# Performance work log

Hardware: AMD Instinct MI355X
Metric: run time of the kernel (lower is better)

Reference implementation:

```python
import jax, jax.numpy as jnp
import numpy as np

N = 8192      # source grid points
M = 8192      # output grid points
NB = 16       # n_basis
WIDTH = 32    # int(n_basis * enhancement)
EPS = 1e-4
LOG2 = 0.6931471805599453


def log_cosh(x):
    a = jnp.abs(x)
    return a + jnp.log1p(jnp.exp(-2.0 * a)) - LOG2


def setup_inputs() -> dict:
    key = jax.random.key(0)
    ks = jax.random.split(key, 9)
    rho = jax.random.uniform(ks[0], (N,), minval=0.05, maxval=2.0)
    gamma = jax.random.uniform(ks[1], (N,), minval=0.01, maxval=1.0)
    coords = jax.random.normal(ks[2], (N, 3)) * 5.0
    weights = jax.random.uniform(ks[3], (N,), minval=0.0, maxval=0.1)
    out_coords = jax.random.normal(ks[4], (M, 3)) * 5.0
    # field_embed params: Linear(1 -> WIDTH), Linear(WIDTH -> NB)
    w1 = jax.random.normal(ks[5], (1, WIDTH)) * 1.0
    b1 = jax.random.normal(ks[6], (WIDTH,)) * 0.1
    w2 = jax.random.normal(ks[7], (WIDTH, NB)) / np.sqrt(WIDTH)
    b2 = jax.random.normal(ks[8], (NB,)) * 0.1
    return {"rho": rho, "gamma": gamma, "coords": coords, "weights": weights,
            "out_coords": out_coords, "w1": w1, "b1": b1, "w2": w2, "b2": b2}


def _field_embed(x, w1, b1, w2, b2):
    # x: (..., 1) -> (..., NB)
    return jnp.tanh(x @ w1 + b1) @ w2 + b2


def reference(rho, gamma, coords, weights, out_coords, w1, b1, w2, b2):
    # rescaled (reduced) density gradient s^2 = gamma / (4 (3 pi^2)^{2/3} rho^{8/3})
    s2 = gamma / (4.0 * (3.0 * jnp.pi ** 2) ** (2.0 / 3.0) * rho ** (8.0 / 3.0))
    x = jnp.log(s2 + EPS)[:, None]                     # (N, 1)
    exponent = log_cosh(_field_embed(x, w1, b1, w2, b2))  # (N, NB)
    heg_scale = log_cosh(_field_embed(jnp.zeros((1, 1), rho.dtype), w1, b1, w2, b2)) ** 1.5  # (1, NB)
    beta = jnp.pi * (rho[:, None] / 2.0) ** (2.0 / 3.0) * exponent  # (N, NB)
    wrho = weights * rho                                # (N,)

    # all-pairs squared distances (M, N), computed once
    d2 = (jnp.sum(out_coords ** 2, axis=1)[:, None]
          + jnp.sum(coords ** 2, axis=1)[None, :]
          - 2.0 * out_coords @ coords.T)
    d2 = jnp.maximum(d2, 0.0)

    # KeOps Genred: y[i, b] = sum_j exp(-beta[j, b] * d2[i, j]) * wrho[j]
    # scan over the (small, fixed) basis axis so only one (M, N) kernel slice lives at a time
    def body(carry, beta_b):                            # beta_b: (N,)
        yb = jnp.exp(-d2 * beta_b[None, :]) @ wrho      # (M,)
        return carry, yb

    _, ys = jax.lax.scan(body, 0, beta.T)               # (NB, M)
    return ys.T * heg_scale                             # (M, NB)
```

## Files before the change

kernel.cpp:

```cpp
#include <hip/hip_runtime.h>
#include <hip/hip_bf16.h>


#define N_PTS 8192
#define M_PTS 8192
#define NBASIS 16
#define WIDTH 32

typedef float v2f __attribute__((ext_vector_type(2)));

__device__ __forceinline__ float exp2_hw(float x) { return __builtin_amdgcn_exp2f(x); }
__device__ __forceinline__ float log2_hw(float x) { return __builtin_amdgcn_logf(x); }

__device__ __forceinline__ float fast_tanh(float z) {
    float a = fabsf(z);
    float t = __expf(-2.0f * a);
    float r = (1.0f - t) / (1.0f + t);
    return copysignf(r, z);
}

__device__ __forceinline__ float log_cosh_f(float x) {
    float a = fabsf(x);
    return a + __logf(1.0f + __expf(-2.0f * a)) - 0.6931471805599453f;
}

__global__ __launch_bounds__(64)
void cg_prep(const float* __restrict__ rho,
             const float* __restrict__ gamma,
             const float* __restrict__ coords,
             const float* __restrict__ weights,
             const float* __restrict__ w1,
             const float* __restrict__ b1,
             const float* __restrict__ w2,
             const float* __restrict__ b2,
             float4* __restrict__ cw,
             float4* __restrict__ bnq,
             float* __restrict__ hegf)
{
    const float PI_F = 3.14159265358979323846f;
    const float LOG2E = 1.4426950408889634f;

    __shared__ float s_w1[WIDTH], s_b1[WIDTH], s_w2[WIDTH * NBASIS], s_b2[NBASIS];
    int t = threadIdx.x;
    if (t < WIDTH) { s_w1[t] = w1[t]; s_b1[t] = b1[t]; }
    if (t < NBASIS) s_b2[t] = b2[t];
    #pragma unroll
    for (int k = 0; k < 8; ++k) s_w2[t + 64 * k] = w2[t + 64 * k];
    __syncthreads();

    int j = blockIdx.x * 64 + t;
    {
        float r = rho[j];
        float g = gamma[j];
        const float c83 = 38.28312007948569f;
        float r83 = exp2_hw(2.6666666667f * log2_hw(r));
        float s2 = g / (c83 * r83);
        float x = __logf(s2 + 1e-4f);

        float emb[NBASIS];
        #pragma unroll
        for (int b = 0; b < NBASIS; ++b) emb[b] = s_b2[b];
        #pragma unroll 4
        for (int w = 0; w < WIDTH; ++w) {
            float h = fast_tanh(fmaf(x, s_w1[w], s_b1[w]));
            #pragma unroll
            for (int b = 0; b < NBASIS; ++b)
                emb[b] = fmaf(h, s_w2[w * NBASIS + b], emb[b]);
        }
        float pref = PI_F * exp2_hw(0.6666666667f * log2_hw(0.5f * r));
        float scale = -LOG2E * pref;
        #pragma unroll
        for (int q = 0; q < 4; ++q) {
            bnq[q * N_PTS + j] = make_float4(scale * log_cosh_f(emb[4 * q + 0]),
                                             scale * log_cosh_f(emb[4 * q + 1]),
                                             scale * log_cosh_f(emb[4 * q + 2]),
                                             scale * log_cosh_f(emb[4 * q + 3]));
        }

        cw[j] = make_float4(coords[j * 3 + 0],
                            coords[j * 3 + 1],
                            coords[j * 3 + 2],
                            weights[j] * r);
    }

    if (blockIdx.x == 0 && t == 0) {
        float emb0[NBASIS];
        #pragma unroll
        for (int b = 0; b < NBASIS; ++b) emb0[b] = s_b2[b];
        for (int w = 0; w < WIDTH; ++w) {
            float h = fast_tanh(s_b1[w]);
            #pragma unroll
            for (int b = 0; b < NBASIS; ++b)
                emb0[b] = fmaf(h, s_w2[w * NBASIS + b], emb0[b]);
        }
        #pragma unroll
        for (int b = 0; b < NBASIS; ++b) {
            float lc = fmaxf(log_cosh_f(emb0[b]), 0.0f);
            hegf[b] = lc * sqrtf(lc);
        }
    }
}

__global__ __launch_bounds__(256, 4)
void cg_pairs(const float* __restrict__ oc,
              const float4* __restrict__ cw,
              const float4* __restrict__ bnq,
              const float* __restrict__ hegf,
              float* __restrict__ out)
{
    int wave = (blockIdx.x << 2) | (threadIdx.x >> 6);
    int lane = threadIdx.x & 63;
    int i0 = wave << 1;
    int i1 = i0 | 1;

    v2f oxv = { oc[i0 * 3 + 0], oc[i1 * 3 + 0] };
    v2f oyv = { oc[i0 * 3 + 1], oc[i1 * 3 + 1] };
    v2f ozv = { oc[i0 * 3 + 2], oc[i1 * 3 + 2] };

    v2f acc[NBASIS];
    #pragma unroll
    for (int b = 0; b < NBASIS; ++b) acc[b] = (v2f)0.0f;

    #pragma unroll 2
    for (int k = 0; k < N_PTS / 64; ++k) {
        int j = (k << 6) | lane;
        float4 c = cw[j];
        v2f dx = oxv - c.x;
        v2f dy = oyv - c.y;
        v2f dz = ozv - c.z;
        v2f d2 = dx * dx + dy * dy + dz * dz;
        #pragma unroll
        for (int q = 0; q < 4; ++q) {
            float4 b4 = bnq[q * N_PTS + j];
            v2f p0 = b4.x * d2;
            v2f p1 = b4.y * d2;
            v2f p2 = b4.z * d2;
            v2f p3 = b4.w * d2;
            v2f e0 = { exp2_hw(p0.x), exp2_hw(p0.y) };
            v2f e1 = { exp2_hw(p1.x), exp2_hw(p1.y) };
            v2f e2 = { exp2_hw(p2.x), exp2_hw(p2.y) };
            v2f e3 = { exp2_hw(p3.x), exp2_hw(p3.y) };
            acc[q * 4 + 0] += e0 * c.w;
            acc[q * 4 + 1] += e1 * c.w;
            acc[q * 4 + 2] += e2 * c.w;
            acc[q * 4 + 3] += e3 * c.w;
        }
    }

    #pragma unroll
    for (int m = 1; m < 64; m <<= 1) {
        #pragma unroll
        for (int b = 0; b < NBASIS; ++b) {
            v2f other = { __shfl_xor(acc[b].x, m, 64),
                          __shfl_xor(acc[b].y, m, 64) };
            acc[b] += other;
        }
    }

    if (lane == 0) {
        #pragma unroll
        for (int b = 0; b < NBASIS; ++b) {
            float h = hegf[b];
            out[i0 * NBASIS + b] = acc[b].x * h;
            out[i1 * NBASIS + b] = acc[b].y * h;
        }
    }
}

extern "C" void kernel_launch(void* const* d_in, const int* in_sizes, int n_in,
                              void* d_out, int out_size, void* d_ws, size_t ws_size,
                              hipStream_t stream) {
    const float* rho        = (const float*)d_in[0];
    const float* gamma      = (const float*)d_in[1];
    const float* coords     = (const float*)d_in[2];
    const float* weights    = (const float*)d_in[3];
    const float* out_coords = (const float*)d_in[4];
    const float* w1         = (const float*)d_in[5];
    const float* b1         = (const float*)d_in[6];
    const float* w2         = (const float*)d_in[7];
    const float* b2         = (const float*)d_in[8];

    char* ws = (char*)d_ws;
    float4* cw   = (float4*)(ws);
    float4* bnq  = (float4*)(ws + (128 << 10));
    float*  hegf = (float*) (ws + (640 << 10));

    cg_prep<<<N_PTS / 64, 64, 0, stream>>>(rho, gamma, coords, weights,
                                           w1, b1, w2, b2,
                                           cw, bnq, hegf);

    cg_pairs<<<M_PTS / 8, 256, 0, stream>>>(out_coords, cw, bnq, hegf,
                                            (float*)d_out);
}
```

Baseline: 189.7 us.

## Offload a quarter of exp2 to FMA polynomial and software-prefetch pair loads

Splits the transcendental load in the pairwise kernel: 12 of 16 basis exponentials still use the hardware exp2 instruction, while the last 4 use a degree-6 polynomial with exponent bit construction on packed FMA units. This is meant to balance the transcendental pipe against the vector ALU. It also double-buffers the coordinate and basis loads one iteration ahead and vectorizes the final output stores. The polynomial adds many ALU instructions and some register pressure, and may lose slight accuracy for very negative arguments where it clamps to tiny values.

```diff
diff --git a/kernel.cpp b/kernel.cpp
--- a/kernel.cpp
+++ b/kernel.cpp
@@ -22,6 +22,24 @@
 __device__ __forceinline__ float log_cosh_f(float x) {
     float a = fabsf(x);
     return a + __logf(1.0f + __expf(-2.0f * a)) - 0.6931471805599453f;
+}
+
+__device__ __forceinline__ v2f exp2_pair_poly(v2f p) {
+    v2f n = { rintf(p.x), rintf(p.y) };
+    v2f r = p - n;
+    int nx = (int)n.x;
+    int ny = (int)n.y;
+    nx = nx < -127 ? -127 : nx;
+    ny = ny < -127 ? -127 : ny;
+    v2f s = { __builtin_bit_cast(float, (nx + 127) << 23),
+              __builtin_bit_cast(float, (ny + 127) << 23) };
+    v2f q = r * 1.535336188319500e-4f + 1.339887440266574e-3f;
+    q = q * r + 9.618437357674640e-3f;
+    q = q * r + 5.550332471162809e-2f;
+    q = q * r + 2.402264791363012e-1f;
+    q = q * r + 6.931472028550421e-1f;
+    q = q * r + 1.0f;
+    return q * s;
 }
 
 __global__ __launch_bounds__(64)
@@ -121,31 +139,62 @@
     #pragma unroll
     for (int b = 0; b < NBASIS; ++b) acc[b] = (v2f)0.0f;
 
-    #pragma unroll 2
-    for (int k = 0; k < N_PTS / 64; ++k) {
-        int j = (k << 6) | lane;
-        float4 c = cw[j];
+    auto hwq = [&](const float4& B, v2f d2, v2f w, int o) {
+        v2f p0 = B.x * d2;
+        v2f p1 = B.y * d2;
+        v2f p2 = B.z * d2;
+        v2f p3 = B.w * d2;
+        v2f e0 = { exp2_hw(p0.x), exp2_hw(p0.y) };
+        v2f e1 = { exp2_hw(p1.x), exp2_hw(p1.y) };
+        v2f e2 = { exp2_hw(p2.x), exp2_hw(p2.y) };
+        v2f e3 = { exp2_hw(p3.x), exp2_hw(p3.y) };
+        acc[o + 0] += e0 * w;
+        acc[o + 1] += e1 * w;
+        acc[o + 2] += e2 * w;
+        acc[o + 3] += e3 * w;
+    };
+    auto polyq = [&](const float4& B, v2f d2, v2f w, int o) {
+        v2f p0 = B.x * d2;
+        v2f p1 = B.y * d2;
+        v2f p2 = B.z * d2;
+        v2f p3 = B.w * d2;
+        acc[o + 0] += exp2_pair_poly(p0) * w;
+        acc[o + 1] += exp2_pair_poly(p1) * w;
+        acc[o + 2] += exp2_pair_poly(p2) * w;
+        acc[o + 3] += exp2_pair_poly(p3) * w;
+    };
+    auto body = [&](const float4& c, const float4& B0, const float4& B1,
+                    const float4& B2, const float4& B3) {
         v2f dx = oxv - c.x;
         v2f dy = oyv - c.y;
         v2f dz = ozv - c.z;
         v2f d2 = dx * dx + dy * dy + dz * dz;
-        #pragma unroll
-        for (int q = 0; q < 4; ++q) {
-            float4 b4 = bnq[q * N_PTS + j];
-            v2f p0 = b4.x * d2;
-            v2f p1 = b4.y * d2;
-            v2f p2 = b4.z * d2;
-            v2f p3 = b4.w * d2;
-            v2f e0 = { exp2_hw(p0.x), exp2_hw(p0.y) };
-            v2f e1 = { exp2_hw(p1.x), exp2_hw(p1.y) };
-            v2f e2 = { exp2_hw(p2.x), exp2_hw(p2.y) };
-            v2f e3 = { exp2_hw(p3.x), exp2_hw(p3.y) };
-            acc[q * 4 + 0] += e0 * c.w;
-            acc[q * 4 + 1] += e1 * c.w;
-            acc[q * 4 + 2] += e2 * c.w;
-            acc[q * 4 + 3] += e3 * c.w;
-        }
-    }
+        v2f w = (v2f)c.w;
+        hwq(B0, d2, w, 0);
+        hwq(B1, d2, w, 4);
+        hwq(B2, d2, w, 8);
+        polyq(B3, d2, w, 12);
+    };
+
+    float4 c_c  = cw[lane];
+    float4 b0_c = bnq[0 * N_PTS + lane];
+    float4 b1_c = bnq[1 * N_PTS + lane];
+    float4 b2_c = bnq[2 * N_PTS + lane];
+    float4 b3_c = bnq[3 * N_PTS + lane];
+
+    for (int k = 0; k < N_PTS / 64 - 1; ++k) {
+        int jn = ((k + 1) << 6) | lane;
+        float4 c_n  = cw[jn];
+        float4 b0_n = bnq[0 * N_PTS + jn];
+        float4 b1_n = bnq[1 * N_PTS + jn];
+        float4 b2_n = bnq[2 * N_PTS + jn];
+        float4 b3_n = bnq[3 * N_PTS + jn];
+
+        body(c_c, b0_c, b1_c, b2_c, b3_c);
+
+        c_c = c_n; b0_c = b0_n; b1_c = b1_n; b2_c = b2_n; b3_c = b3_n;
+    }
+    body(c_c, b0_c, b1_c, b2_c, b3_c);
 
     #pragma unroll
     for (int m = 1; m < 64; m <<= 1) {
@@ -158,11 +207,18 @@
     }
 
     if (lane == 0) {
-        #pragma unroll
-        for (int b = 0; b < NBASIS; ++b) {
-            float h = hegf[b];
-            out[i0 * NBASIS + b] = acc[b].x * h;
-            out[i1 * NBASIS + b] = acc[b].y * h;
+        float4* o0 = (float4*)(out + i0 * NBASIS);
+        float4* o1 = (float4*)(out + i1 * NBASIS);
+        #pragma unroll
+        for (int q = 0; q < 4; ++q) {
+            float h0 = hegf[4 * q + 0];
+            float h1 = hegf[4 * q + 1];
+            float h2 = hegf[4 * q + 2];
+            float h3 = hegf[4 * q + 3];
+            o0[q] = make_float4(acc[4 * q + 0].x * h0, acc[4 * q + 1].x * h1,
+                                acc[4 * q + 2].x * h2, acc[4 * q + 3].x * h3);
+            o1[q] = make_float4(acc[4 * q + 0].y * h0, acc[4 * q + 1].y * h1,
+                                acc[4 * q + 2].y * h2, acc[4 * q + 3].y * h3);
         }
     }
 }
```

Measured after the change: 236.4 us. +24.7%, slower.

## Morton-sort points and skip negligible exp groups via wave-uniform cutoff

Applied to the files above, without the earlier changes.

Adds a binning kernel that sorts source and output points by a 16^3 Morton key. Sorted points make each wave's 64 sources and 2 targets spatially coherent. The pair kernel then uses a per-source maximum exponent to skip whole groups of four basis exponentials when every lane's exponent is below -17. This is meant to drop exp2 work for distant pairs, at the cost of a small truncation error, an extra serial sort kernel, and divergent-branch overhead. Output stores are also vectorised to float4.

```diff
diff --git a/kernel.cpp b/kernel.cpp
--- a/kernel.cpp
+++ b/kernel.cpp
@@ -6,6 +6,7 @@
 #define M_PTS 8192
 #define NBASIS 16
 #define WIDTH 32
+#define NBINS 4096
 
 typedef float v2f __attribute__((ext_vector_type(2)));
 
@@ -22,6 +23,61 @@
 __device__ __forceinline__ float log_cosh_f(float x) {
     float a = fabsf(x);
     return a + __logf(1.0f + __expf(-2.0f * a)) - 0.6931471805599453f;
+}
+
+__global__ __launch_bounds__(1024)
+void cg_bin(const float* __restrict__ coords,
+            const float* __restrict__ out_coords,
+            unsigned* __restrict__ jperm,
+            unsigned* __restrict__ iperm)
+{
+    const float* pts = (blockIdx.x == 0) ? coords : out_coords;
+    unsigned* perm   = (blockIdx.x == 0) ? jperm : iperm;
+
+    __shared__ unsigned short s_key[N_PTS];
+    __shared__ unsigned s_hist[NBINS];
+    __shared__ unsigned s_tmp[NBINS];
+    int t = threadIdx.x;
+
+    for (int e = t; e < NBINS; e += 1024) s_hist[e] = 0;
+    __syncthreads();
+
+    for (int e = t; e < N_PTS; e += 1024) {
+        float x = pts[e * 3 + 0];
+        float y = pts[e * 3 + 1];
+        float z = pts[e * 3 + 2];
+        int xi = (int)((x + 24.0f) * 0.3333333f); xi = xi < 0 ? 0 : (xi > 15 ? 15 : xi);
+        int yi = (int)((y + 24.0f) * 0.3333333f); yi = yi < 0 ? 0 : (yi > 15 ? 15 : yi);
+        int zi = (int)((z + 24.0f) * 0.3333333f); zi = zi < 0 ? 0 : (zi > 15 ? 15 : zi);
+        unsigned key = 0;
+        #pragma unroll
+        for (int k = 0; k < 4; ++k) {
+            key |= ((unsigned)((xi >> k) & 1)) << (3 * k + 2);
+            key |= ((unsigned)((yi >> k) & 1)) << (3 * k + 1);
+            key |= ((unsigned)((zi >> k) & 1)) << (3 * k + 0);
+        }
+        s_key[e] = (unsigned short)key;
+        atomicAdd(&s_hist[key], 1u);
+    }
+    __syncthreads();
+
+    #pragma unroll
+    for (int step = 0; step < 12; ++step) {
+        int d = 1 << step;
+        unsigned* src = (step & 1) ? s_tmp : s_hist;
+        unsigned* dst = (step & 1) ? s_hist : s_tmp;
+        for (int e = t; e < NBINS; e += 1024)
+            dst[e] = src[e] + (e >= d ? src[e - d] : 0u);
+        __syncthreads();
+    }
+    for (int e = t; e < NBINS; e += 1024)
+        s_tmp[e] = (e == 0) ? 0u : s_hist[e - 1];
+    __syncthreads();
+
+    for (int e = t; e < N_PTS; e += 1024) {
+        unsigned pos = atomicAdd(&s_tmp[s_key[e]], 1u);
+        perm[pos] = (unsigned)e;
+    }
 }
 
 __global__ __launch_bounds__(64)
@@ -33,8 +89,10 @@
              const float* __restrict__ b1,
              const float* __restrict__ w2,
              const float* __restrict__ b2,
+             const unsigned* __restrict__ jperm,
              float4* __restrict__ cw,
              float4* __restrict__ bnq,
+             float4* __restrict__ bmx,
              float* __restrict__ hegf)
 {
     const float PI_F = 3.14159265358979323846f;
@@ -48,7 +106,8 @@
     for (int k = 0; k < 8; ++k) s_w2[t + 64 * k] = w2[t + 64 * k];
     __syncthreads();
 
-    int j = blockIdx.x * 64 + t;
+    int kdst = blockIdx.x * 64 + t;
+    int j = (int)jperm[kdst];
     {
         float r = rho[j];
         float g = gamma[j];
@@ -69,18 +128,22 @@
         }
         float pref = PI_F * exp2_hw(0.6666666667f * log2_hw(0.5f * r));
         float scale = -LOG2E * pref;
+        float pmax[4];
         #pragma unroll
         for (int q = 0; q < 4; ++q) {
-            bnq[q * N_PTS + j] = make_float4(scale * log_cosh_f(emb[4 * q + 0]),
-                                             scale * log_cosh_f(emb[4 * q + 1]),
-                                             scale * log_cosh_f(emb[4 * q + 2]),
-                                             scale * log_cosh_f(emb[4 * q + 3]));
-        }
-
-        cw[j] = make_float4(coords[j * 3 + 0],
-                            coords[j * 3 + 1],
-                            coords[j * 3 + 2],
-                            weights[j] * r);
+            float b0 = scale * log_cosh_f(emb[4 * q + 0]);
+            float b1v = scale * log_cosh_f(emb[4 * q + 1]);
+            float b2v = scale * log_cosh_f(emb[4 * q + 2]);
+            float b3 = scale * log_cosh_f(emb[4 * q + 3]);
+            bnq[q * N_PTS + kdst] = make_float4(b0, b1v, b2v, b3);
+            pmax[q] = fmaxf(fmaxf(b0, b1v), fmaxf(b2v, b3));
+        }
+        bmx[kdst] = make_float4(pmax[0], pmax[1], pmax[2], pmax[3]);
+
+        cw[kdst] = make_float4(coords[j * 3 + 0],
+                               coords[j * 3 + 1],
+                               coords[j * 3 + 2],
+                               weights[j] * r);
     }
 
     if (blockIdx.x == 0 && t == 0) {
@@ -105,13 +168,16 @@
 void cg_pairs(const float* __restrict__ oc,
               const float4* __restrict__ cw,
               const float4* __restrict__ bnq,
+              const float4* __restrict__ bmx,
+              const unsigned* __restrict__ iperm,
               const float* __restrict__ hegf,
               float* __restrict__ out)
 {
+    const float SKIP = -17.0f;
     int wave = (blockIdx.x << 2) | (threadIdx.x >> 6);
     int lane = threadIdx.x & 63;
-    int i0 = wave << 1;
-    int i1 = i0 | 1;
+    int i0 = (int)iperm[wave << 1];
+    int i1 = (int)iperm[(wave << 1) | 1];
 
     v2f oxv = { oc[i0 * 3 + 0], oc[i1 * 3 + 0] };
     v2f oyv = { oc[i0 * 3 + 1], oc[i1 * 3 + 1] };
@@ -125,25 +191,56 @@
     for (int k = 0; k < N_PTS / 64; ++k) {
         int j = (k << 6) | lane;
         float4 c = cw[j];
+        float4 bm = bmx[j];
         v2f dx = oxv - c.x;
         v2f dy = oyv - c.y;
         v2f dz = ozv - c.z;
         v2f d2 = dx * dx + dy * dy + dz * dz;
-        #pragma unroll
-        for (int q = 0; q < 4; ++q) {
-            float4 b4 = bnq[q * N_PTS + j];
-            v2f p0 = b4.x * d2;
-            v2f p1 = b4.y * d2;
-            v2f p2 = b4.z * d2;
-            v2f p3 = b4.w * d2;
-            v2f e0 = { exp2_hw(p0.x), exp2_hw(p0.y) };
-            v2f e1 = { exp2_hw(p1.x), exp2_hw(p1.y) };
-            v2f e2 = { exp2_hw(p2.x), exp2_hw(p2.y) };
-            v2f e3 = { exp2_hw(p3.x), exp2_hw(p3.y) };
-            acc[q * 4 + 0] += e0 * c.w;
-            acc[q * 4 + 1] += e1 * c.w;
-            acc[q * 4 + 2] += e2 * c.w;
-            acc[q * 4 + 3] += e3 * c.w;
+        float4 B0 = bnq[0 * N_PTS + j];
+        float4 B1 = bnq[1 * N_PTS + j];
+        float4 B2 = bnq[2 * N_PTS + j];
+        float4 B3 = bnq[3 * N_PTS + j];
+        float bmw = fmaxf(fmaxf(bm.x, bm.y), fmaxf(bm.z, bm.w));
+        v2f pw = bmw * d2;
+        if (!__all((pw.x <= SKIP) && (pw.y <= SKIP))) {
+            v2f w = (v2f)c.w;
+            v2f pm;
+            pm = bm.x * d2;
+            if (!__all((pm.x <= SKIP) && (pm.y <= SKIP))) {
+                v2f p0 = B0.x * d2, p1 = B0.y * d2, p2 = B0.z * d2, p3 = B0.w * d2;
+                v2f e0 = { exp2_hw(p0.x), exp2_hw(p0.y) };
+                v2f e1 = { exp2_hw(p1.x), exp2_hw(p1.y) };
+                v2f e2 = { exp2_hw(p2.x), exp2_hw(p2.y) };
+                v2f e3 = { exp2_hw(p3.x), exp2_hw(p3.y) };
+                acc[0] += e0 * w; acc[1] += e1 * w; acc[2] += e2 * w; acc[3] += e3 * w;
+            }
+            pm = bm.y * d2;
+            if (!__all((pm.x <= SKIP) && (pm.y <= SKIP))) {
+                v2f p0 = B1.x * d2, p1 = B1.y * d2, p2 = B1.z * d2, p3 = B1.w * d2;
+                v2f e0 = { exp2_hw(p0.x), exp2_hw(p0.y) };
+                v2f e1 = { exp2_hw(p1.x), exp2_hw(p1.y) };
+                v2f e2 = { exp2_hw(p2.x), exp2_hw(p2.y) };
+                v2f e3 = { exp2_hw(p3.x), exp2_hw(p3.y) };
+                acc[4] += e0 * w; acc[5] += e1 * w; acc[6] += e2 * w; acc[7] += e3 * w;
+            }
+            pm = bm.z * d2;
+            if (!__all((pm.x <= SKIP) && (pm.y <= SKIP))) {
+                v2f p0 = B2.x * d2, p1 = B2.y * d2, p2 = B2.z * d2, p3 = B2.w * d2;
+                v2f e0 = { exp2_hw(p0.x), exp2_hw(p0.y) };
+                v2f e1 = { exp2_hw(p1.x), exp2_hw(p1.y) };
+                v2f e2 = { exp2_hw(p2.x), exp2_hw(p2.y) };
+                v2f e3 = { exp2_hw(p3.x), exp2_hw(p3.y) };
+                acc[8] += e0 * w; acc[9] += e1 * w; acc[10] += e2 * w; acc[11] += e3 * w;
+            }
+            pm = bm.w * d2;
+            if (!__all((pm.x <= SKIP) && (pm.y <= SKIP))) {
+                v2f p0 = B3.x * d2, p1 = B3.y * d2, p2 = B3.z * d2, p3 = B3.w * d2;
+                v2f e0 = { exp2_hw(p0.x), exp2_hw(p0.y) };
+                v2f e1 = { exp2_hw(p1.x), exp2_hw(p1.y) };
+                v2f e2 = { exp2_hw(p2.x), exp2_hw(p2.y) };
+                v2f e3 = { exp2_hw(p3.x), exp2_hw(p3.y) };
+                acc[12] += e0 * w; acc[13] += e1 * w; acc[14] += e2 * w; acc[15] += e3 * w;
+            }
         }
     }
 
@@ -158,11 +255,18 @@
     }
 
     if (lane == 0) {
-        #pragma unroll
-        for (int b = 0; b < NBASIS; ++b) {
-            float h = hegf[b];
-            out[i0 * NBASIS + b] = acc[b].x * h;
-            out[i1 * NBASIS + b] = acc[b].y * h;
+        float4* o0 = (float4*)(out + i0 * NBASIS);
+        float4* o1 = (float4*)(out + i1 * NBASIS);
+        #pragma unroll
+        for (int q = 0; q < 4; ++q) {
+            float h0 = hegf[4 * q + 0];
+            float h1 = hegf[4 * q + 1];
+            float h2 = hegf[4 * q + 2];
+            float h3 = hegf[4 * q + 3];
+            o0[q] = make_float4(acc[4 * q + 0].x * h0, acc[4 * q + 1].x * h1,
+                                acc[4 * q + 2].x * h2, acc[4 * q + 3].x * h3);
+            o1[q] = make_float4(acc[4 * q + 0].y * h0, acc[4 * q + 1].y * h1,
+                                acc[4 * q + 2].y * h2, acc[4 * q + 3].y * h3);
         }
     }
 }
@@ -181,14 +285,19 @@
     const float* b2         = (const float*)d_in[8];
 
     char* ws = (char*)d_ws;
-    float4* cw   = (float4*)(ws);
-    float4* bnq  = (float4*)(ws + (128 << 10));
-    float*  hegf = (float*) (ws + (640 << 10));
+    float4*   cw    = (float4*)(ws);
+    float4*   bnq   = (float4*)(ws + (128 << 10));
+    float4*   bmx   = (float4*)(ws + (640 << 10));
+    float*    hegf  = (float*)  (ws + (768 << 10));
+    unsigned* jperm = (unsigned*)(ws + (772 << 10));
+    unsigned* iperm = (unsigned*)(ws + (804 << 10));
+
+    cg_bin<<<2, 1024, 0, stream>>>(coords, out_coords, jperm, iperm);
 
     cg_prep<<<N_PTS / 64, 64, 0, stream>>>(rho, gamma, coords, weights,
-                                           w1, b1, w2, b2,
-                                           cw, bnq, hegf);
-
-    cg_pairs<<<M_PTS / 8, 256, 0, stream>>>(out_coords, cw, bnq, hegf,
-                                            (float*)d_out);
-}
+                                           w1, b1, w2, b2, jperm,
+                                           cw, bnq, bmx, hegf);
+
+    cg_pairs<<<M_PTS / 8, 256, 0, stream>>>(out_coords, cw, bnq, bmx, iperm,
+                                            hegf, (float*)d_out);
+}
```

New measurement: 318.3 us. 67.8% more time.
